# Kernel optimization log

Hardware: AMD Instinct MI355X
Metric: run time of the kernel (lower is better)

Reference implementation:

```python
import jax, jax.numpy as jnp
import numpy as np

B, S, H, V = 32, 512, 1024, 8192


def setup_inputs() -> dict:
    key = jax.random.key(0)
    ks = jax.random.split(key, 12)
    def g(k, shape, scale):
        return jax.random.normal(k, shape, dtype=jnp.float32) * scale
    sH = 1.0 / float(np.sqrt(H))
    s2H = 1.0 / float(np.sqrt(2 * H))
    return {
        "encoder_output": g(ks[0], (B, S, H), 1.0),
        "h0": g(ks[1], (B, H), 1.0),
        "c0": g(ks[2], (B, H), 1.0),
        "context_vec": jnp.zeros((B, S, H), jnp.float32),
        "W_ih": g(ks[3], (4 * H, 2 * H), s2H),
        "b_ih": jnp.zeros((4 * H,), jnp.float32),
        "W_hh": g(ks[4], (4 * H, H), sH),
        "b_hh": jnp.zeros((4 * H,), jnp.float32),
        "attn_l1_w": g(ks[5], (H, H), sH),
        "attn_l2_w": g(ks[6], (H, 2 * H), s2H),
        "lin1_w": g(ks[7], (H, H), sH),
        "lin1_b": jnp.zeros((H,), jnp.float32),
        "lin2_w": g(ks[8], (V, H), sH),
        "lin2_b": jnp.zeros((V,), jnp.float32),
        "xs_len": jax.random.randint(ks[9], (B,), 1, S + 1),
    }


def reference(encoder_output, h0, c0, context_vec, W_ih, b_ih, W_hh, b_hh,
              attn_l1_w, attn_l2_w, lin1_w, lin1_b, lin2_w, lin2_b, xs_len):
    # mask[b,s] = 1 if s < xs_len[b]
    mask = (jnp.arange(S)[None, :] < xs_len[:, None]).astype(encoder_output.dtype)  # [B,S]
    enc_t = jnp.swapaxes(encoder_output, 0, 1)   # [S,B,H]
    ctx_t = jnp.swapaxes(context_vec, 0, 1)      # [S,B,H]

    def step(carry, xt):
        h, c = carry
        e, cv = xt
        # LSTMCell with input = concat(encoder step, context step) of size 2H
        inp = jnp.concatenate([e, cv], axis=-1)                       # [B,2H]
        gates = inp @ W_ih.T + b_ih + h @ W_hh.T + b_hh               # [B,4H]
        i, f, g, o = jnp.split(gates, 4, axis=-1)
        c_new = jax.nn.sigmoid(f) * c + jax.nn.sigmoid(i) * jnp.tanh(g)
        h_new = jax.nn.sigmoid(o) * jnp.tanh(c_new)
        # masked bmm attention over encoder outputs
        q = h_new @ attn_l1_w.T                                       # [B,H]
        score = jnp.einsum('bsh,bh->bs', encoder_output, q)           # [B,S]
        m = mask * score
        m = jnp.where(m == 0, -1e10, m)                               # masked_att[masked_att==0] = -1e10
        attn = jax.nn.softmax(m, axis=1)                              # [B,S]
        ctx = jnp.einsum('bs,bsh->bh', attn, encoder_output)          # [B,H]
        ctx = jnp.tanh(jnp.concatenate([ctx, h_new], axis=-1) @ attn_l2_w.T)
        # output MLP + log-softmax
        sc = jnp.tanh(ctx @ lin1_w.T + lin1_b) @ lin2_w.T + lin2_b    # [B,V]
        sc = jax.nn.log_softmax(sc, axis=1)
        return (h_new, c_new), sc

    (_, _), scores = jax.lax.scan(step, (h0, c0), (enc_t, ctx_t))
    return jnp.swapaxes(scores, 0, 1)  # [B,S,V]
```

## Files before the change

kernel.cpp:

```cpp
#include <hip/hip_runtime.h>
#include <math.h>

#define B_  32
#define S_  512
#define H_  1024
#define V_  8192
#define G4_ 4096
#define H2_ 2048

template<int TRANSB>
__global__ __launch_bounds__(256)
void sgemm_kernel(const float* __restrict__ A1, const float* __restrict__ A2,
                  const float* __restrict__ Bm,
                  const float* __restrict__ bias1, const float* __restrict__ bias2,
                  float* __restrict__ C,
                  int M, int N, int K1, int K2, int ldb, int ldc,
                  long sA, long sB, long sC, int act)
{
    __shared__ float As[16][132];
    __shared__ float Bs[16][132];
    const int tid = threadIdx.x;
    const int n0 = blockIdx.x * 128;
    const int m0 = blockIdx.y * 128;
    const int z  = blockIdx.z;
    const float* A1z = A1 + (long)z * sA;
    const float* A2z = A2;
    const float* Bz  = Bm + (long)z * sB;
    float*       Cz  = C  + (long)z * sC;

    const int K  = K1 + K2;
    const int tx = tid & 15, ty = tid >> 4;

    float acc[8][8];
#pragma unroll
    for (int i = 0; i < 8; i++)
#pragma unroll
        for (int j = 0; j < 8; j++) acc[i][j] = 0.f;

    for (int k0 = 0; k0 < K; k0 += 16) {
#pragma unroll
        for (int q = 0; q < 2; q++) {
            int L   = q * 256 + tid;
            int mm  = L >> 2;
            int kk4 = (L & 3) << 2;
            int gk  = k0 + kk4;
            float4 v;
            if (gk < K1) v = *(const float4*)(A1z + (long)(m0 + mm) * K1 + gk);
            else         v = *(const float4*)(A2z + (long)(m0 + mm) * K2 + (gk - K1));
            As[kk4 + 0][mm] = v.x; As[kk4 + 1][mm] = v.y;
            As[kk4 + 2][mm] = v.z; As[kk4 + 3][mm] = v.w;
        }
        if (TRANSB) {
#pragma unroll
            for (int q = 0; q < 2; q++) {
                int L   = q * 256 + tid;
                int nn  = L >> 2;
                int kk4 = (L & 3) << 2;
                float4 v = *(const float4*)(Bz + (long)(n0 + nn) * ldb + k0 + kk4);
                Bs[kk4 + 0][nn] = v.x; Bs[kk4 + 1][nn] = v.y;
                Bs[kk4 + 2][nn] = v.z; Bs[kk4 + 3][nn] = v.w;
            }
        } else {
#pragma unroll
            for (int q = 0; q < 2; q++) {
                int L   = q * 256 + tid;
                int kk  = L >> 5;
                int nn4 = (L & 31) << 2;
                float4 v = *(const float4*)(Bz + (long)(k0 + kk) * ldb + n0 + nn4);
                *(float4*)&Bs[kk][nn4] = v;
            }
        }
        __syncthreads();
#pragma unroll
        for (int kk = 0; kk < 16; kk++) {
            float a[8], b[8];
            *(float4*)&a[0] = *(const float4*)&As[kk][ty * 8];
            *(float4*)&a[4] = *(const float4*)&As[kk][ty * 8 + 4];
            *(float4*)&b[0] = *(const float4*)&Bs[kk][tx * 8];
            *(float4*)&b[4] = *(const float4*)&Bs[kk][tx * 8 + 4];
#pragma unroll
            for (int i = 0; i < 8; i++)
#pragma unroll
                for (int j = 0; j < 8; j++)
                    acc[i][j] = fmaf(a[i], b[j], acc[i][j]);
        }
        __syncthreads();
    }
#pragma unroll
    for (int i = 0; i < 8; i++) {
        long gm = m0 + ty * 8 + i;
#pragma unroll
        for (int j4 = 0; j4 < 2; j4++) {
            int gn = n0 + tx * 8 + j4 * 4;
            float4 v;
            v.x = acc[i][j4 * 4 + 0]; v.y = acc[i][j4 * 4 + 1];
            v.z = acc[i][j4 * 4 + 2]; v.w = acc[i][j4 * 4 + 3];
            if (bias1) { v.x += bias1[gn + 0]; v.y += bias1[gn + 1];
                         v.z += bias1[gn + 2]; v.w += bias1[gn + 3]; }
            if (bias2) { v.x += bias2[gn + 0]; v.y += bias2[gn + 1];
                         v.z += bias2[gn + 2]; v.w += bias2[gn + 3]; }
            if (act == 1) { v.x = tanhf(v.x); v.y = tanhf(v.y);
                            v.z = tanhf(v.z); v.w = tanhf(v.w); }
            *(float4*)(Cz + gm * ldc + gn) = v;
        }
    }
}

__global__ __launch_bounds__(256, 1)
void lstm_step_kernel(const float* __restrict__ gpre, const float* __restrict__ Whh,
                      const float* __restrict__ hprev, long hstride,
                      const float* __restrict__ cprev,
                      float* __restrict__ cnext, float* __restrict__ hall_t,
                      int t)
{
    __shared__ float hs[64 * 132];
    const int tid = threadIdx.x;
    const int bid = blockIdx.x;
    const int rr  = tid & 3;
    const int c   = tid >> 2;

    float wreg[4][16];
#pragma unroll
    for (int m = 0; m < 4; m++) {
        const float* wr = Whh + (long)(rr * 1024 + bid * 4 + m) * 1024;
#pragma unroll
        for (int q = 0; q < 4; q++) {
            float4 v = *(const float4*)(wr + q * 256 + c * 4);
            wreg[m][q * 4 + 0] = v.x; wreg[m][q * 4 + 1] = v.y;
            wreg[m][q * 4 + 2] = v.z; wreg[m][q * 4 + 3] = v.w;
        }
    }

    float acc[4][32];
#pragma unroll
    for (int m = 0; m < 4; m++)
#pragma unroll
        for (int b = 0; b < 32; b++) acc[m][b] = 0.f;

#pragma unroll
    for (int q = 0; q < 4; q++) {
        {
            int g  = tid & 63;
            int bq = tid >> 6;
#pragma unroll
            for (int v4 = 0; v4 < 8; v4++) {
                int b = bq * 8 + v4;
                float4 v = *(const float4*)(hprev + (long)b * hstride + q * 256 + g * 4);
                *(float4*)&hs[g * 132 + b * 4] = v;
            }
        }
        __syncthreads();
#pragma unroll
        for (int b = 0; b < 32; b++) {
            float4 h4 = *(const float4*)&hs[c * 132 + b * 4];
#pragma unroll
            for (int m = 0; m < 4; m++) {
                acc[m][b] = fmaf(wreg[m][q * 4 + 0], h4.x, acc[m][b]);
                acc[m][b] = fmaf(wreg[m][q * 4 + 1], h4.y, acc[m][b]);
                acc[m][b] = fmaf(wreg[m][q * 4 + 2], h4.z, acc[m][b]);
                acc[m][b] = fmaf(wreg[m][q * 4 + 3], h4.w, acc[m][b]);
            }
        }
        __syncthreads();
    }

#pragma unroll
    for (int m = 0; m < 4; m++)
#pragma unroll
        for (int b = 0; b < 32; b++) {
            float v = acc[m][b];
            v += __shfl_xor(v, 4);
            v += __shfl_xor(v, 8);
            v += __shfl_xor(v, 16);
            v += __shfl_xor(v, 32);
            acc[m][b] = v;
        }

    int w = tid >> 6;
    if ((tid & 63) < 4) {
        int r2 = tid & 3;
#pragma unroll
        for (int m = 0; m < 4; m++)
#pragma unroll
            for (int b = 0; b < 32; b++)
                hs[(w * 16 + r2 * 4 + m) * 33 + b] = acc[m][b];
    }
    __syncthreads();

    if (tid < 128) {
        int jj = tid >> 5;
        int b  = tid & 31;
        float gv[4];
#pragma unroll
        for (int g = 0; g < 4; g++) {
            int lr = g * 4 + jj;
            float s = hs[(0 * 16 + lr) * 33 + b] + hs[(1 * 16 + lr) * 33 + b]
                    + hs[(2 * 16 + lr) * 33 + b] + hs[(3 * 16 + lr) * 33 + b];
            gv[g] = s + gpre[((long)b * S_ + t) * G4_ + g * H_ + bid * 4 + jj];
        }
        int col = bid * 4 + jj;
        float cp = cprev[b * H_ + col];
        float ig = 1.f / (1.f + expf(-gv[0]));
        float fg = 1.f / (1.f + expf(-gv[1]));
        float gg = tanhf(gv[2]);
        float og = 1.f / (1.f + expf(-gv[3]));
        float cn = fg * cp + ig * gg;
        float hn = og * tanhf(cn);
        cnext[b * H_ + col] = cn;
        hall_t[(long)b * (S_ * H_) + col] = hn;
    }
}

__device__ __forceinline__ float wave_max(float v) {
    v = fmaxf(v, __shfl_xor(v, 1));  v = fmaxf(v, __shfl_xor(v, 2));
    v = fmaxf(v, __shfl_xor(v, 4));  v = fmaxf(v, __shfl_xor(v, 8));
    v = fmaxf(v, __shfl_xor(v, 16)); v = fmaxf(v, __shfl_xor(v, 32));
    return v;
}
__device__ __forceinline__ float wave_sum(float v) {
    v += __shfl_xor(v, 1);  v += __shfl_xor(v, 2);
    v += __shfl_xor(v, 4);  v += __shfl_xor(v, 8);
    v += __shfl_xor(v, 16); v += __shfl_xor(v, 32);
    return v;
}

__global__ __launch_bounds__(256)
void masked_softmax_kernel(float* __restrict__ sc, const int* __restrict__ xs)
{
    __shared__ float red[4];
    int row = blockIdx.x;
    int b   = row >> 9;
    int len = xs[b];
    float* p = sc + (long)row * S_;
    int tid = threadIdx.x;
    float v0 = p[tid];
    float v1 = p[tid + 256];
    v0 = (tid < len) ? v0 : 0.f;       if (v0 == 0.f) v0 = -1e10f;
    v1 = (tid + 256 < len) ? v1 : 0.f; if (v1 == 0.f) v1 = -1e10f;
    float m = wave_max(fmaxf(v0, v1));
    if ((tid & 63) == 0) red[tid >> 6] = m;
    __syncthreads();
    m = fmaxf(fmaxf(red[0], red[1]), fmaxf(red[2], red[3]));
    float e0 = expf(v0 - m), e1 = expf(v1 - m);
    float s = wave_sum(e0 + e1);
    __syncthreads();
    if ((tid & 63) == 0) red[tid >> 6] = s;
    __syncthreads();
    s = red[0] + red[1] + red[2] + red[3];
    float inv = 1.f / s;
    p[tid] = e0 * inv;
    p[tid + 256] = e1 * inv;
}

__global__ __launch_bounds__(256)
void log_softmax_kernel(float* __restrict__ out)
{
    __shared__ float red[4];
    long row = blockIdx.x;
    float* p = out + row * V_;
    int tid = threadIdx.x;
    float x[32];
#pragma unroll
    for (int i = 0; i < 8; i++)
        *(float4*)&x[i * 4] = *(const float4*)(p + i * 1024 + tid * 4);
    float m = -INFINITY;
#pragma unroll
    for (int i = 0; i < 32; i++) m = fmaxf(m, x[i]);
    m = wave_max(m);
    if ((tid & 63) == 0) red[tid >> 6] = m;
    __syncthreads();
    m = fmaxf(fmaxf(red[0], red[1]), fmaxf(red[2], red[3]));
    float s = 0.f;
#pragma unroll
    for (int i = 0; i < 32; i++) s += expf(x[i] - m);
    s = wave_sum(s);
    __syncthreads();
    if ((tid & 63) == 0) red[tid >> 6] = s;
    __syncthreads();
    s = red[0] + red[1] + red[2] + red[3];
    float lse = m + logf(s);
#pragma unroll
    for (int i = 0; i < 8; i++) {
        float4 v;
        v.x = x[i * 4 + 0] - lse; v.y = x[i * 4 + 1] - lse;
        v.z = x[i * 4 + 2] - lse; v.w = x[i * 4 + 3] - lse;
        *(float4*)(p + i * 1024 + tid * 4) = v;
    }
}

extern "C" void kernel_launch(void* const* d_in, const int* in_sizes, int n_in,
                              void* d_out, int out_size, void* d_ws, size_t ws_size,
                              hipStream_t stream)
{
    const float* enc  = (const float*)d_in[0];
    const float* h0   = (const float*)d_in[1];
    const float* c0   = (const float*)d_in[2];
    const float* cv   = (const float*)d_in[3];
    const float* W_ih = (const float*)d_in[4];
    const float* b_ih = (const float*)d_in[5];
    const float* W_hh = (const float*)d_in[6];
    const float* b_hh = (const float*)d_in[7];
    const float* al1  = (const float*)d_in[8];
    const float* al2  = (const float*)d_in[9];
    const float* l1w  = (const float*)d_in[10];
    const float* l1b  = (const float*)d_in[11];
    const float* l2w  = (const float*)d_in[12];
    const float* l2b  = (const float*)d_in[13];
    const int*   xs   = (const int*)d_in[14];
    float* out = (float*)d_out;

    float* gpre    = out;
    float* qbuf    = out + 67108864;
    float* scoresb = out + 83886080;
    float* hall    = out + 92274688;
    float* ctxbuf  = gpre;
    float* ctx2buf = qbuf;

    float* ws    = (float*)d_ws;
    float* t1buf = ws;
    float* cws   = ws + 16777216;

    dim3 blk(256);

    sgemm_kernel<1><<<dim3(G4_ / 128, 16384 / 128, 1), blk, 0, stream>>>(
        enc, cv, W_ih, b_ih, b_hh, gpre,
        16384, G4_, H_, H_, H2_, G4_, 0, 0, 0, 0);

    for (int t = 0; t < S_; t++) {
        const float* hp = t ? hall + (long)(t - 1) * H_ : h0;
        long hstr       = t ? (long)S_ * H_ : (long)H_;
        const float* cp = t ? (const float*)cws : c0;
        lstm_step_kernel<<<256, blk, 0, stream>>>(
            gpre, W_hh, hp, hstr, cp, cws, hall + (long)t * H_, t);
    }

    sgemm_kernel<1><<<dim3(H_ / 128, 16384 / 128, 1), blk, 0, stream>>>(
        hall, nullptr, al1, nullptr, nullptr, qbuf,
        16384, H_, H_, 0, H_, H_, 0, 0, 0, 0);

    sgemm_kernel<1><<<dim3(S_ / 128, S_ / 128, B_), blk, 0, stream>>>(
        qbuf, nullptr, enc, nullptr, nullptr, scoresb,
        S_, S_, H_, 0, H_, S_, (long)S_ * H_, (long)S_ * H_, (long)S_ * S_, 0);

    masked_softmax_kernel<<<16384, blk, 0, stream>>>(scoresb, xs);

    sgemm_kernel<0><<<dim3(H_ / 128, S_ / 128, B_), blk, 0, stream>>>(
        scoresb, nullptr, enc, nullptr, nullptr, ctxbuf,
        S_, H_, S_, 0, H_, H_, (long)S_ * S_, (long)S_ * H_, (long)S_ * H_, 0);

    sgemm_kernel<1><<<dim3(H_ / 128, 16384 / 128, 1), blk, 0, stream>>>(
        ctxbuf, hall, al2, nullptr, nullptr, ctx2buf,
        16384, H_, H_, H_, H2_, H_, 0, 0, 0, 1);

    sgemm_kernel<1><<<dim3(H_ / 128, 16384 / 128, 1), blk, 0, stream>>>(
        ctx2buf, nullptr, l1w, l1b, nullptr, t1buf,
        16384, H_, H_, 0, H_, H_, 0, 0, 0, 1);

    sgemm_kernel<1><<<dim3(V_ / 128, 16384 / 128, 1), blk, 0, stream>>>(
        t1buf, nullptr, l2w, l2b, nullptr, out,
        16384, V_, H_, 0, H_, V_, 0, 0, 0, 0);

    log_softmax_kernel<<<16384, blk, 0, stream>>>(out);
}
```

Measured before the change: 18.84 ms.

## Use bf16 MFMA GEMM kernel for output projection layers

Adds a bf16 MFMA-based NT GEMM kernel that converts fp32 tiles to bf16 in shared memory and uses 16x16x32 bf16 matrix instructions. It replaces the three scalar fp32 SGEMMs for attn_l2, lin1 and lin2 (the largest being 16384x8192x1024). The goal is to move the dominant output-projection FLOPs onto matrix cores. The tradeoff is reduced precision in these layers and an unpipelined, single-buffered load loop.

```diff
diff --git a/kernel.cpp b/kernel.cpp
--- a/kernel.cpp
+++ b/kernel.cpp
@@ -102,6 +102,98 @@
             if (act == 1) { v.x = tanhf(v.x); v.y = tanhf(v.y);
                             v.z = tanhf(v.z); v.w = tanhf(v.w); }
             *(float4*)(Cz + gm * ldc + gn) = v;
+        }
+    }
+}
+
+typedef short v8s __attribute__((ext_vector_type(8)));
+typedef float v4f __attribute__((ext_vector_type(4)));
+
+__device__ __forceinline__ ushort f2bf(float x) {
+    unsigned u = __float_as_uint(x);
+    return (ushort)((u + 0x7FFFu + ((u >> 16) & 1u)) >> 16);
+}
+
+__global__ __launch_bounds__(256)
+void bgemm_nt_kernel(const float* __restrict__ A1, const float* __restrict__ A2,
+                     const float* __restrict__ B,
+                     const float* __restrict__ bias,
+                     float* __restrict__ C,
+                     int K1, int K2, int ldc, int act)
+{
+    constexpr int LDK = 40;
+    __shared__ __align__(16) ushort As[128 * LDK];
+    __shared__ __align__(16) ushort Bs[128 * LDK];
+    const int tid = threadIdx.x;
+    const int n0 = blockIdx.x * 128;
+    const int m0 = blockIdx.y * 128;
+    const int K  = K1 + K2;
+
+    const int l  = tid & 63;
+    const int w  = tid >> 6;
+    const int wm = (w >> 1) * 64;
+    const int wn = (w & 1) * 64;
+    const int fr = l & 15;
+    const int ko = (l >> 4) * 8;
+
+    const int srow = tid >> 3;
+    const int skc  = (tid & 7) * 4;
+
+    v4f acc[4][4];
+#pragma unroll
+    for (int i = 0; i < 4; i++)
+#pragma unroll
+        for (int j = 0; j < 4; j++)
+#pragma unroll
+            for (int r = 0; r < 4; r++) acc[i][j][r] = 0.f;
+
+    for (int k0 = 0; k0 < K; k0 += 32) {
+        const float* Az; int kb, lda;
+        if (k0 < K1) { Az = A1; kb = k0;      lda = K1; }
+        else         { Az = A2; kb = k0 - K1; lda = K2; }
+#pragma unroll
+        for (int p = 0; p < 4; p++) {
+            int r = srow + p * 32;
+            float4 va = *(const float4*)(Az + (long)(m0 + r) * lda + kb + skc);
+            ushort4 pa;
+            pa.x = f2bf(va.x); pa.y = f2bf(va.y); pa.z = f2bf(va.z); pa.w = f2bf(va.w);
+            *(ushort4*)&As[r * LDK + skc] = pa;
+            float4 vb = *(const float4*)(B + (long)(n0 + r) * K + k0 + skc);
+            ushort4 pb;
+            pb.x = f2bf(vb.x); pb.y = f2bf(vb.y); pb.z = f2bf(vb.z); pb.w = f2bf(vb.w);
+            *(ushort4*)&Bs[r * LDK + skc] = pb;
+        }
+        __syncthreads();
+        v8s av[4], bv[4];
+#pragma unroll
+        for (int i = 0; i < 4; i++)
+            av[i] = *(const v8s*)&As[(wm + i * 16 + fr) * LDK + ko];
+#pragma unroll
+        for (int j = 0; j < 4; j++)
+            bv[j] = *(const v8s*)&Bs[(wn + j * 16 + fr) * LDK + ko];
+#pragma unroll
+        for (int i = 0; i < 4; i++)
+#pragma unroll
+            for (int j = 0; j < 4; j++)
+                acc[i][j] = __builtin_amdgcn_mfma_f32_16x16x32_bf16(
+                    av[i], bv[j], acc[i][j], 0, 0, 0);
+        __syncthreads();
+    }
+
+    const int orow = (l >> 4) * 4;
+#pragma unroll
+    for (int i = 0; i < 4; i++) {
+#pragma unroll
+        for (int j = 0; j < 4; j++) {
+            int col = n0 + wn + j * 16 + fr;
+            float bb = bias ? bias[col] : 0.f;
+#pragma unroll
+            for (int r = 0; r < 4; r++) {
+                long row = m0 + wm + i * 16 + orow + r;
+                float v = acc[i][j][r] + bb;
+                if (act == 1) v = tanhf(v);
+                C[row * (long)ldc + col] = v;
+            }
         }
     }
 }
@@ -348,17 +440,14 @@
         scoresb, nullptr, enc, nullptr, nullptr, ctxbuf,
         S_, H_, S_, 0, H_, H_, (long)S_ * S_, (long)S_ * H_, (long)S_ * H_, 0);
 
-    sgemm_kernel<1><<<dim3(H_ / 128, 16384 / 128, 1), blk, 0, stream>>>(
-        ctxbuf, hall, al2, nullptr, nullptr, ctx2buf,
-        16384, H_, H_, H_, H2_, H_, 0, 0, 0, 1);
-
-    sgemm_kernel<1><<<dim3(H_ / 128, 16384 / 128, 1), blk, 0, stream>>>(
-        ctx2buf, nullptr, l1w, l1b, nullptr, t1buf,
-        16384, H_, H_, 0, H_, H_, 0, 0, 0, 1);
-
-    sgemm_kernel<1><<<dim3(V_ / 128, 16384 / 128, 1), blk, 0, stream>>>(
-        t1buf, nullptr, l2w, l2b, nullptr, out,
-        16384, V_, H_, 0, H_, V_, 0, 0, 0, 0);
+    bgemm_nt_kernel<<<dim3(H_ / 128, 16384 / 128), blk, 0, stream>>>(
+        ctxbuf, hall, al2, nullptr, ctx2buf, H_, H_, H_, 1);
+
+    bgemm_nt_kernel<<<dim3(H_ / 128, 16384 / 128), blk, 0, stream>>>(
+        ctx2buf, nullptr, l1w, l1b, t1buf, H_, 0, H_, 1);
+
+    bgemm_nt_kernel<<<dim3(V_ / 128, 16384 / 128), blk, 0, stream>>>(
+        t1buf, nullptr, l2w, l2b, out, H_, 0, V_, 0);
 
     log_softmax_kernel<<<16384, blk, 0, stream>>>(out);
 }
```

Result: faster. 15.21 ms (-19.3%).
